# Performance work log

Measured on AMD Instinct MI355X. Metric: run time of the kernel, lower is better.

Reference implementation:

```python
import jax, jax.numpy as jnp
import numpy as np

N_NODES = 10000
N_EDGES = 160000
IN_DIM, HID_DIM, OUT_DIM = 256, 512, 256


def gcn_conv(x, W, b, src, dst, dinv):
    # PyG GCNConv with add_self_loops=True and symmetric normalization.
    # dinv = deg^{-1/2} computed once (degrees include self loops).
    h = x @ W                                   # [N, F_out]
    norm = dinv[src] * dinv[dst]                # [E]
    msg = h[src] * norm[:, None]                # gather + scale, [E, F_out]
    agg = jnp.zeros_like(h).at[dst].add(msg)    # scatter-add over edges
    agg = agg + h * (dinv * dinv)[:, None]      # self-loop contribution
    return agg + b


def setup_inputs() -> dict:
    key = jax.random.key(0)
    ks = jax.random.split(key, 8)
    x = jax.random.normal(ks[0], (N_NODES, IN_DIM), dtype=jnp.float32)
    edge_index = jax.random.randint(ks[1], (2, N_EDGES), 0, N_NODES, dtype=jnp.int64)

    def glorot(k, fan_in, fan_out):
        s = jnp.sqrt(6.0 / (fan_in + fan_out)).astype(jnp.float32)
        return jax.random.uniform(k, (fan_in, fan_out), jnp.float32, -s, s)

    return {
        "x": x,
        "W1": glorot(ks[2], IN_DIM, HID_DIM), "b1": jnp.zeros((HID_DIM,), jnp.float32),
        "W2": glorot(ks[3], HID_DIM, HID_DIM), "b2": jnp.zeros((HID_DIM,), jnp.float32),
        "W3": glorot(ks[4], HID_DIM, OUT_DIM), "b3": jnp.zeros((OUT_DIM,), jnp.float32),
        "edge_index": edge_index,
    }


def reference(x, W1, b1, W2, b2, W3, b3, edge_index):
    src, dst = edge_index[0], edge_index[1]
    n = x.shape[0]
    # degree with self loops (edge weight 1), shared by all three layers
    deg = jnp.zeros((n,), x.dtype).at[dst].add(1.0) + 1.0
    dinv = jax.lax.rsqrt(deg)
    h = jnp.tanh(gcn_conv(x, W1, b1, src, dst, dinv))
    h = jnp.tanh(gcn_conv(h, W2, b2, src, dst, dinv))
    out = gcn_conv(h, W3, b3, src, dst, dinv)
    return out
```

## Files before the change

kernel.cpp:

```cpp
#include <hip/hip_runtime.h>
#include <math.h>

#define NN 10000
#define NE 160000
#define IN_DIM 256
#define HID_DIM 512
#define OUT_DIM 256

typedef unsigned short u16;
typedef _Float16 f16x8 __attribute__((ext_vector_type(8)));
typedef __attribute__((ext_vector_type(4))) float f32x4;


union F16U { _Float16 h; u16 u; };
static __device__ __forceinline__ u16 f2h_bits(float f) {
    F16U v; v.h = (_Float16)f; return v.u;
}


__global__ void k_init(const float* __restrict__ W1, const float* __restrict__ W2,
                       const float* __restrict__ W3, const float* __restrict__ x,
                       u16* __restrict__ W1h, u16* __restrict__ W1l,
                       u16* __restrict__ W2h, u16* __restrict__ W2l,
                       u16* __restrict__ W3h, u16* __restrict__ W3l,
                       u16* __restrict__ xh, int* __restrict__ deg) {
    int idx = blockIdx.x * blockDim.x + threadIdx.x;
    const int S1 = IN_DIM * HID_DIM;
    const int S2 = HID_DIM * HID_DIM;
    const int S3 = HID_DIM * OUT_DIM;
    const int TW = S1 + S2 + S3;
    const int TX = NN * IN_DIM;
    if (idx < TW) {
        const float* W; u16 *Th, *Tl; int K, N, local;
        if (idx < S1)           { W = W1; Th = W1h; Tl = W1l; K = IN_DIM;  N = HID_DIM; local = idx; }
        else if (idx < S1 + S2) { W = W2; Th = W2h; Tl = W2l; K = HID_DIM; N = HID_DIM; local = idx - S1; }
        else                    { W = W3; Th = W3h; Tl = W3l; K = HID_DIM; N = OUT_DIM; local = idx - S1 - S2; }
        int k = local / N, n = local - k * N;
        float v = W[local];
        F16U hh; hh.h = (_Float16)v;
        float r = (v - (float)hh.h) * 2048.0f;
        Th[(size_t)n * K + k] = hh.u;
        Tl[(size_t)n * K + k] = f2h_bits(r);
    } else if (idx < TW + TX) {
        int j = idx - TW;
        xh[j] = f2h_bits(x[j]);
    } else if (idx < TW + TX + NN) {
        deg[idx - TW - TX] = 0;
    }
}


__global__ void k_count_deg(const int* __restrict__ dst, int* __restrict__ deg) {
    int e = blockIdx.x * blockDim.x + threadIdx.x;
    if (e < NE) atomicAdd(&deg[dst[e]], 1);
}

__launch_bounds__(1024)
__global__ void k_scan(const int* __restrict__ deg, int* __restrict__ row,
                       int* __restrict__ csr, float* __restrict__ dinv) {
    __shared__ int sdeg[10240];
    __shared__ int sums[1024];
    const int tid = threadIdx.x;
    for (int i = tid; i < NN; i += 1024) sdeg[i] = deg[i];
    __syncthreads();
    const int CH = 10;
    int base = tid * CH;
    int s = 0;
    for (int j = 0; j < CH; ++j) {
        int i = base + j;
        if (i < NN) s += sdeg[i] + 1;
    }
    sums[tid] = s;
    __syncthreads();
    for (int off = 1; off < 1024; off <<= 1) {
        int t = (tid >= off) ? sums[tid - off] : 0;
        __syncthreads();
        sums[tid] += t;
        __syncthreads();
    }
    int run = sums[tid] - s;
    for (int j = 0; j < CH; ++j) {
        int i = base + j;
        if (i < NN) {
            int dg = sdeg[i];
            csr[run] = i;
            row[i] = run + 1;
            dinv[i] = rsqrtf((float)dg + 1.0f);
            run += dg + 1;
        }
    }
}

__global__ void k_fill(const int* __restrict__ src, const int* __restrict__ dst,
                       int* __restrict__ row, int* __restrict__ csr) {
    int e = blockIdx.x * blockDim.x + threadIdx.x;
    if (e < NE) {
        int pos = atomicAdd(&row[dst[e]], 1);
        csr[pos] = src[e];
    }
}


struct PfSet { uint4 a0, a1, bh, bl; };

template<int K, bool HAS_BIAS, bool DO_TANH, bool F16_OUT, bool ROWSCALE>
__launch_bounds__(256)
__global__ void k_gemm_f16x2(const u16* __restrict__ A, const u16* __restrict__ Bhi,
                             const u16* __restrict__ Blo,
                             const float* __restrict__ bias, const float* __restrict__ rowscale,
                             float* __restrict__ C, u16* __restrict__ Ch,
                             int M, int N, int MT, int MT8) {
    __shared__ uint4 As[2][512];
    __shared__ uint4 BsH[2][256];
    __shared__ uint4 BsL[2][256];

    const int id = blockIdx.x;
    const int xcd = id & 7;
    const int q2 = id >> 3;
    const int mt = (q2 % MT8) * 8 + xcd;
    const int nt = q2 / MT8;
    if (mt >= MT) return;

    const int tid  = threadIdx.x;
    const int wave = tid >> 6;
    const int lane = tid & 63;
    const int lr   = lane & 15;
    const int quad = lane >> 4;
    const int m_base = mt * 128;
    const int n_base = nt * 64;

    const int s_row = tid >> 2;
    const int s_kq  = tid & 3;
    const int c_lo  = ((s_row >> 4) << 6) + s_kq * 16 + (s_row & 15);

    const u16* pA0 = A   + (size_t)(m_base + s_row) * K + s_kq * 8;
    const u16* pA1 = pA0 + (size_t)64 * K;
    const u16* pBh = Bhi + (size_t)(n_base + s_row) * K + s_kq * 8;
    const u16* pBl = Blo + (size_t)(n_base + s_row) * K + s_kq * 8;
    const bool g0 = (m_base + s_row) < M;
    const bool g1 = (m_base + s_row + 64) < M;

    const uint4 z = make_uint4(0u, 0u, 0u, 0u);

    auto load_set = [&](int it, PfSet& r) {
        const int ko = it * 32;
        r.a0 = z; r.a1 = z;
        if (g0) r.a0 = *(const uint4*)(pA0 + ko);
        if (g1) r.a1 = *(const uint4*)(pA1 + ko);
        r.bh = *(const uint4*)(pBh + ko);
        r.bl = *(const uint4*)(pBl + ko);
    };
    auto lds_write = [&](int buf, const PfSet& r) {
        As[buf][c_lo] = r.a0;
        As[buf][c_lo + 256] = r.a1;
        BsH[buf][c_lo] = r.bh;
        BsL[buf][c_lo] = r.bl;
    };

    f32x4 accH[2][4] = {};
    f32x4 accL[2][4] = {};

    auto compute = [&](int buf) {
        f16x8 a[2], bH[4], bL[4];
#pragma unroll
        for (int tm = 0; tm < 2; ++tm) {
            int c = (wave * 2 + tm) * 64 + lane;
            a[tm] = *(const f16x8*)&As[buf][c];
        }
#pragma unroll
        for (int tn = 0; tn < 4; ++tn) {
            int c = tn * 64 + lane;
            bH[tn] = *(const f16x8*)&BsH[buf][c];
            bL[tn] = *(const f16x8*)&BsL[buf][c];
        }
#pragma unroll
        for (int tm = 0; tm < 2; ++tm)
#pragma unroll
            for (int tn = 0; tn < 4; ++tn) {
                accH[tm][tn] = __builtin_amdgcn_mfma_f32_16x16x32_f16(a[tm], bH[tn], accH[tm][tn], 0, 0, 0);
                accL[tm][tn] = __builtin_amdgcn_mfma_f32_16x16x32_f16(a[tm], bL[tn], accL[tm][tn], 0, 0, 0);
            }
    };

    const int NIT = K >> 5;
    PfSet sA;

    load_set(0, sA);
    lds_write(0, sA);
    __syncthreads();

    for (int it = 0; it < NIT; ++it) {
        const bool has_next = (it + 1) < NIT;
        PfSet sN;
        if (has_next) load_set(it + 1, sN);
        compute(it & 1);
        if (has_next) lds_write((it + 1) & 1, sN);
        __syncthreads();
    }

#pragma unroll
    for (int tm = 0; tm < 2; ++tm) {
        int row0 = m_base + wave * 32 + tm * 16 + quad * 4;
#pragma unroll
        for (int i = 0; i < 4; ++i) {
            int row = row0 + i;
            if (row >= M) continue;
            float rs = ROWSCALE ? rowscale[row] : 1.0f;
#pragma unroll
            for (int tn = 0; tn < 4; ++tn) {
                int col = n_base + tn * 16 + lr;
                float v = accH[tm][tn][i] + accL[tm][tn][i] * (1.0f / 2048.0f);
                if (HAS_BIAS) v += bias[col];
                if (DO_TANH) v = tanhf(v);
                if (ROWSCALE) v *= rs;
                if (F16_OUT) {
                    Ch[(size_t)row * N + col] = f2h_bits(v);
                } else {
                    C[(size_t)row * N + col] = v;
                }
            }
        }
    }
}


template<bool PRESCALED, bool HAS_BIAS, bool F16_OUT, int F>
__launch_bounds__(256)
__global__ void k_gather_h(const u16* __restrict__ h, const float* __restrict__ dinv,
                           const int* __restrict__ row_end, const int* __restrict__ csr,
                           const float* __restrict__ bias,
                           float* __restrict__ outF, u16* __restrict__ outH) {
    constexpr int L  = F / 8;
    constexpr int LS = L / 8;
    constexpr int NPB = 256 / LS;
    const int tid = threadIdx.x;
    const int d = (blockIdx.x >> 3) * NPB + tid / LS;
    if (d >= NN) return;
    const int f8 = (blockIdx.x & 7) * LS + (tid & (LS - 1));

    const int start = (d == 0) ? 0 : row_end[d - 1];
    const int end = row_end[d];
    const uint4* h16 = (const uint4*)h;

    float acc[8] = {};
    int e = start;
    for (; e + 8 <= end; e += 8) {
        int s[8]; uint4 raw[8]; float w[8];
#pragma unroll
        for (int j = 0; j < 8; ++j) s[j] = csr[e + j];
#pragma unroll
        for (int j = 0; j < 8; ++j) raw[j] = h16[(size_t)s[j] * L + f8];
#pragma unroll
        for (int j = 0; j < 8; ++j) w[j] = PRESCALED ? 1.0f : dinv[s[j]];
#pragma unroll
        for (int j = 0; j < 8; ++j) {
            f16x8 hv = *(const f16x8*)&raw[j];
#pragma unroll
            for (int t = 0; t < 8; ++t) acc[t] += w[j] * (float)hv[t];
        }
    }
    for (; e < end; ++e) {
        int s = csr[e];
        float w = PRESCALED ? 1.0f : dinv[s];
        uint4 raw = h16[(size_t)s * L + f8];
        f16x8 hv = *(const f16x8*)&raw;
#pragma unroll
        for (int t = 0; t < 8; ++t) acc[t] += w * (float)hv[t];
    }

    const float dd = dinv[d];
    float r[8];
#pragma unroll
    for (int t = 0; t < 8; ++t) r[t] = dd * acc[t];
    if (HAS_BIAS) {
        const float4* b4 = (const float4*)bias;
        float4 b0 = b4[f8 * 2], b1 = b4[f8 * 2 + 1];
        r[0] += b0.x; r[1] += b0.y; r[2] += b0.z; r[3] += b0.w;
        r[4] += b1.x; r[5] += b1.y; r[6] += b1.z; r[7] += b1.w;
    }
    if (F16_OUT) {
        union { u16 a[8]; uint4 v; } pk;
#pragma unroll
        for (int t = 0; t < 8; ++t) pk.a[t] = f2h_bits(r[t]);
        ((uint4*)outH)[(size_t)d * L + f8] = pk.v;
    } else {
        size_t base = (size_t)d * (F / 4) + f8 * 2;
        ((float4*)outF)[base]     = make_float4(r[0], r[1], r[2], r[3]);
        ((float4*)outF)[base + 1] = make_float4(r[4], r[5], r[6], r[7]);
    }
}


extern "C" void kernel_launch(void* const* d_in, const int* in_sizes, int n_in,
                              void* d_out, int out_size, void* d_ws, size_t ws_size,
                              hipStream_t stream) {
    const float* x  = (const float*)d_in[0];
    const float* W1 = (const float*)d_in[1];
    const float* b1 = (const float*)d_in[2];
    const float* W2 = (const float*)d_in[3];
    const float* b2 = (const float*)d_in[4];
    const float* W3 = (const float*)d_in[5];
    const float* b3 = (const float*)d_in[6];
    const int* edge = (const int*)d_in[7];
    const int* src = edge;
    const int* dst = edge + NE;
    float* out = (float*)d_out;

    const size_t SLOT = (size_t)NN * HID_DIM * 4;
    char* p = (char*)d_ws;
    char* slot0 = p;
    char* slot1 = p + SLOT;
    char* q = p + 2 * SLOT;
    u16* W1Th = (u16*)q; q += (size_t)IN_DIM  * HID_DIM * 2;
    u16* W1Tl = (u16*)q; q += (size_t)IN_DIM  * HID_DIM * 2;
    u16* W2Th = (u16*)q; q += (size_t)HID_DIM * HID_DIM * 2;
    u16* W2Tl = (u16*)q; q += (size_t)HID_DIM * HID_DIM * 2;
    u16* W3Th = (u16*)q; q += (size_t)HID_DIM * OUT_DIM * 2;
    u16* W3Tl = (u16*)q; q += (size_t)HID_DIM * OUT_DIM * 2;
    int*   deg  = (int*)q;   q += (size_t)NN * 4;
    float* dinv = (float*)q; q += (size_t)NN * 4;
    int*   row  = (int*)q;   q += (size_t)NN * 4;
    int*   csr  = (int*)q;   q += (size_t)(NE + NN) * 4;
    u16*   xh   = (u16*)q;   q += (size_t)NN * IN_DIM * 2;

    u16* Xagg  = (u16*)slot0;
    u16* g1h   = (u16*)slot1;
    u16* H1agg = (u16*)slot0;
    u16* h2    = (u16*)slot1;
    u16* g3h   = (u16*)slot0;

    const int T = 256;
    const int MT = (NN + 127) / 128;
    const int MT8 = (MT + 7) / 8;

    {
        int total = IN_DIM * HID_DIM + HID_DIM * HID_DIM + HID_DIM * OUT_DIM
                  + NN * IN_DIM + NN;
        k_init<<<(total + T - 1) / T, T, 0, stream>>>(W1, W2, W3, x, W1Th, W1Tl,
                                                      W2Th, W2Tl, W3Th, W3Tl, xh, deg);
    }
    k_count_deg<<<(NE + T - 1) / T, T, 0, stream>>>(dst, deg);
    k_scan<<<1, 1024, 0, stream>>>(deg, row, csr, dinv);
    k_fill<<<(NE + T - 1) / T, T, 0, stream>>>(src, dst, row, csr);

    const int G256 = ((NN + 63) / 64) * 8;
    const int G512 = ((NN + 31) / 32) * 8;
    const int GEMM_G512 = 8 * MT8 * (HID_DIM / 64);
    const int GEMM_G256 = 8 * MT8 * (OUT_DIM / 64);

    k_gather_h<false, false, true, IN_DIM><<<G256, 256, 0, stream>>>(
        xh, dinv, row, csr, nullptr, nullptr, Xagg);
    k_gemm_f16x2<IN_DIM, true, true, true, true><<<GEMM_G512, 256, 0, stream>>>(
        Xagg, W1Th, W1Tl, b1, dinv, nullptr, g1h, NN, HID_DIM, MT, MT8);

    k_gather_h<true, false, true, HID_DIM><<<G512, 256, 0, stream>>>(
        g1h, dinv, row, csr, nullptr, nullptr, H1agg);
    k_gemm_f16x2<HID_DIM, true, true, true, false><<<GEMM_G512, 256, 0, stream>>>(
        H1agg, W2Th, W2Tl, b2, nullptr, nullptr, h2, NN, HID_DIM, MT, MT8);

    k_gemm_f16x2<HID_DIM, false, false, true, true><<<GEMM_G256, 256, 0, stream>>>(
        h2, W3Th, W3Tl, nullptr, dinv, nullptr, g3h, NN, OUT_DIM, MT, MT8);
    k_gather_h<true, true, false, OUT_DIM><<<G256, 256, 0, stream>>>(
        g3h, dinv, row, csr, b3, out, nullptr);

    (void)in_sizes; (void)n_in; (void)out_size; (void)ws_size;
}
```

Baseline: 227.7 us.

## Stage GEMM tiles via direct global-to-LDS loads and use a 2x2 wave tiling

The f16x2 GEMM now copies A, Bhi and Blo tiles straight from global memory into LDS with global_load_lds. This replaces the old path that prefetched into registers and then wrote to LDS, which saves VGPRs and LDS store instructions. The wave layout also changes from 1x4 (each wave 32 rows x 64 cols) to 2x2 (64 rows x 32 cols), which changes how many A and B fragments each wave reads from LDS. The row bound guards on A loads are gone, so the last M tile may read past row M unless the buffer is padded.

```diff
diff --git a/kernel.cpp b/kernel.cpp
--- a/kernel.cpp
+++ b/kernel.cpp
@@ -15,6 +15,12 @@
 union F16U { _Float16 h; u16 u; };
 static __device__ __forceinline__ u16 f2h_bits(float f) {
     F16U v; v.h = (_Float16)f; return v.u;
+}
+
+static __device__ __forceinline__ void gload_lds(const u16* g, uint4* l) {
+    __builtin_amdgcn_global_load_lds((const __attribute__((address_space(1))) void*)g,
+                                     (__attribute__((address_space(3))) void*)l,
+                                     16, 0, 0);
 }
 
 
@@ -101,8 +107,6 @@
 }
 
 
-struct PfSet { uint4 a0, a1, bh, bl; };
-
 template<int K, bool HAS_BIAS, bool DO_TANH, bool F16_OUT, bool ROWSCALE>
 __launch_bounds__(256)
 __global__ void k_gemm_f16x2(const u16* __restrict__ A, const u16* __restrict__ Bhi,
@@ -126,89 +130,68 @@
     const int lane = tid & 63;
     const int lr   = lane & 15;
     const int quad = lane >> 4;
+    const int wm   = wave >> 1;
+    const int wn   = wave & 1;
     const int m_base = mt * 128;
     const int n_base = nt * 64;
 
-    const int s_row = tid >> 2;
-    const int s_kq  = tid & 3;
-    const int c_lo  = ((s_row >> 4) << 6) + s_kq * 16 + (s_row & 15);
-
-    const u16* pA0 = A   + (size_t)(m_base + s_row) * K + s_kq * 8;
-    const u16* pA1 = pA0 + (size_t)64 * K;
-    const u16* pBh = Bhi + (size_t)(n_base + s_row) * K + s_kq * 8;
-    const u16* pBl = Blo + (size_t)(n_base + s_row) * K + s_kq * 8;
-    const bool g0 = (m_base + s_row) < M;
-    const bool g1 = (m_base + s_row + 64) < M;
-
-    const uint4 z = make_uint4(0u, 0u, 0u, 0u);
-
-    auto load_set = [&](int it, PfSet& r) {
+    const u16* gA  = A   + (size_t)(m_base + wave * 32 + lr) * K + quad * 8;
+    const u16* gBh = Bhi + (size_t)(n_base + wave * 16 + lr) * K + quad * 8;
+    const u16* gBl = Blo + (size_t)(n_base + wave * 16 + lr) * K + quad * 8;
+
+    auto stage = [&](int buf, int it) {
         const int ko = it * 32;
-        r.a0 = z; r.a1 = z;
-        if (g0) r.a0 = *(const uint4*)(pA0 + ko);
-        if (g1) r.a1 = *(const uint4*)(pA1 + ko);
-        r.bh = *(const uint4*)(pBh + ko);
-        r.bl = *(const uint4*)(pBl + ko);
+        gload_lds(gA  + ko,          &As [buf][wave * 128]);
+        gload_lds(gA  + ko + 16 * K, &As [buf][wave * 128 + 64]);
+        gload_lds(gBh + ko,          &BsH[buf][wave * 64]);
+        gload_lds(gBl + ko,          &BsL[buf][wave * 64]);
     };
-    auto lds_write = [&](int buf, const PfSet& r) {
-        As[buf][c_lo] = r.a0;
-        As[buf][c_lo + 256] = r.a1;
-        BsH[buf][c_lo] = r.bh;
-        BsL[buf][c_lo] = r.bl;
-    };
-
-    f32x4 accH[2][4] = {};
-    f32x4 accL[2][4] = {};
+
+    f32x4 accH[4][2] = {};
+    f32x4 accL[4][2] = {};
 
     auto compute = [&](int buf) {
-        f16x8 a[2], bH[4], bL[4];
-#pragma unroll
-        for (int tm = 0; tm < 2; ++tm) {
-            int c = (wave * 2 + tm) * 64 + lane;
-            a[tm] = *(const f16x8*)&As[buf][c];
-        }
-#pragma unroll
-        for (int tn = 0; tn < 4; ++tn) {
-            int c = tn * 64 + lane;
+        f16x8 a[4], bH[2], bL[2];
+#pragma unroll
+        for (int tn = 0; tn < 2; ++tn) {
+            int c = (wn * 2 + tn) * 64 + lane;
             bH[tn] = *(const f16x8*)&BsH[buf][c];
             bL[tn] = *(const f16x8*)&BsL[buf][c];
         }
 #pragma unroll
-        for (int tm = 0; tm < 2; ++tm)
-#pragma unroll
-            for (int tn = 0; tn < 4; ++tn) {
+        for (int tm = 0; tm < 4; ++tm)
+            a[tm] = *(const f16x8*)&As[buf][(wm * 4 + tm) * 64 + lane];
+#pragma unroll
+        for (int tm = 0; tm < 4; ++tm)
+#pragma unroll
+            for (int tn = 0; tn < 2; ++tn) {
                 accH[tm][tn] = __builtin_amdgcn_mfma_f32_16x16x32_f16(a[tm], bH[tn], accH[tm][tn], 0, 0, 0);
                 accL[tm][tn] = __builtin_amdgcn_mfma_f32_16x16x32_f16(a[tm], bL[tn], accL[tm][tn], 0, 0, 0);
             }
     };
 
     const int NIT = K >> 5;
-    PfSet sA;
-
-    load_set(0, sA);
-    lds_write(0, sA);
+
+    stage(0, 0);
     __syncthreads();
 
     for (int it = 0; it < NIT; ++it) {
-        const bool has_next = (it + 1) < NIT;
-        PfSet sN;
-        if (has_next) load_set(it + 1, sN);
+        if (it + 1 < NIT) stage((it + 1) & 1, it + 1);
         compute(it & 1);
-        if (has_next) lds_write((it + 1) & 1, sN);
         __syncthreads();
     }
 
 #pragma unroll
-    for (int tm = 0; tm < 2; ++tm) {
-        int row0 = m_base + wave * 32 + tm * 16 + quad * 4;
+    for (int tm = 0; tm < 4; ++tm) {
+        int row0 = m_base + wm * 64 + tm * 16 + quad * 4;
 #pragma unroll
         for (int i = 0; i < 4; ++i) {
             int row = row0 + i;
             if (row >= M) continue;
             float rs = ROWSCALE ? rowscale[row] : 1.0f;
 #pragma unroll
-            for (int tn = 0; tn < 4; ++tn) {
-                int col = n_base + tn * 16 + lr;
+            for (int tn = 0; tn < 2; ++tn) {
+                int col = n_base + wn * 32 + tn * 16 + lr;
                 float v = accH[tm][tn][i] + accL[tm][tn][i] * (1.0f / 2048.0f);
                 if (HAS_BIAS) v += bias[col];
                 if (DO_TANH) v = tanhf(v);
```

After: 238.3 us. +4.7%, slower.
